# Performance work log

Measured on AMD Instinct MI355X. Metric: run time of the kernel, lower is better.

The kernel has to match this reference:

```python
import jax, jax.numpy as jnp
import numpy as np

B, T, I, H, A = 1024, 2048, 8, 256, 8
DT = 0.1
EPS = 1e-5

def _layernorm(x, g, b):
    m = jnp.mean(x, axis=-1, keepdims=True)
    v = jnp.mean(jnp.square(x - m), axis=-1, keepdims=True)
    return (x - m) * jax.lax.rsqrt(v + EPS) * g + b

def setup_inputs() -> dict:
    key = jax.random.key(0)
    ks = jax.random.split(key, 8)
    xav = float(np.sqrt(6.0 / (H + H)))  # xavier_uniform for rec_weights
    return {
        "x": jax.random.normal(ks[0], (B, T, I), dtype=jnp.float32),
        "W_in": jax.random.normal(ks[1], (I, H), dtype=jnp.float32) * (1.0 / np.sqrt(I)),
        "b_in": jnp.zeros((H,), dtype=jnp.float32),
        "tau_param": jnp.ones((H,), dtype=jnp.float32),
        "W_rec": jax.random.uniform(ks[2], (H, H), dtype=jnp.float32, minval=-xav, maxval=xav),
        "g1": jnp.ones((H,), dtype=jnp.float32),
        "beta1": jnp.zeros((H,), dtype=jnp.float32),
        "g2": jnp.ones((H,), dtype=jnp.float32),
        "beta2": jnp.zeros((H,), dtype=jnp.float32),
        "head_w": jax.random.normal(ks[3], (H, A), dtype=jnp.float32) * (1.0 / np.sqrt(H)),
        "head_b": jnp.zeros((A,), dtype=jnp.float32),
    }

def reference(x, W_in, b_in, tau_param, W_rec, g1, beta1, g2, beta2, head_w, head_b):
    tau = jax.nn.softplus(tau_param)  # [H], broadcast over batch
    # Precompute input projection for all timesteps in one GEMM: [B,T,H]
    u = jnp.einsum("bti,ih->bth", x, W_in) + b_in
    u_t = jnp.swapaxes(u, 0, 1)  # [T,B,H] for scan

    def step(h, u_step):
        f = jnp.tanh(_layernorm(u_step + h @ W_rec, g1, beta1))
        h = jnp.clip(h + (-h / tau + f) * DT, -10.0, 10.0)
        return h, None

    h0 = jnp.zeros((x.shape[0], W_rec.shape[0]), dtype=x.dtype)
    h, _ = jax.lax.scan(step, h0, u_t)
    # per-appliance linear heads, fused into one matmul: [B, A]
    return _layernorm(h, g2, beta2) @ head_w + head_b
```

## Files before the change

### kernel.cpp

```cpp
#include <hip/hip_runtime.h>
#include <hip/hip_bf16.h>

#define T_ 2048
#define B_ 1024
#define H_ 256
#define I_ 8
#define A_ 8
#define DT_ 0.1f
#define EPS_ 1e-5f
#define LSTR 296
#define CH 32
#define RB 8

typedef __attribute__((ext_vector_type(8))) short bf16x8;
typedef __attribute__((ext_vector_type(4))) float f32x4;

#if __has_builtin(__builtin_amdgcn_cvt_pk_bf16_f32)
typedef __attribute__((ext_vector_type(2))) __bf16 bf16x2;
__device__ __forceinline__ int pk2bf(float a, float b) {
    bf16x2 r = __builtin_amdgcn_cvt_pk_bf16_f32(a, b);
    return __builtin_bit_cast(int, r);
}
#else
__device__ __forceinline__ short f2bf1(float f) {
    unsigned u = __builtin_bit_cast(unsigned, f);
    u += 0x7fffu + ((u >> 16) & 1u);
    return (short)(u >> 16);
}
__device__ __forceinline__ int pk2bf(float a, float b) {
    return (int)(unsigned short)f2bf1(a) | ((int)f2bf1(b) << 16);
}
#endif

__launch_bounds__(512, 2)
__global__ void liquid_kernel(const float* __restrict__ x,
                              const float* __restrict__ W_in,
                              const float* __restrict__ b_in,
                              const float* __restrict__ tau_param,
                              const float* __restrict__ W_rec,
                              const float* __restrict__ g1,
                              const float* __restrict__ beta1,
                              const float* __restrict__ g2,
                              const float* __restrict__ beta2,
                              const float* __restrict__ head_w,
                              const float* __restrict__ head_b,
                              float* __restrict__ out) {
    __shared__ short  h_lds[RB * LSTR];
    __shared__ short  xstage[2][CH][RB][8];
    __shared__ alignas(16) int zero16[4];
    __shared__ alignas(16) float2 redt[RB][10];
    __shared__ float  hw[H_ * A_];
    __shared__ float  outp[8][RB][A_];

    const int tid  = threadIdx.x;
    const int w    = tid >> 6;
    const int lane = tid & 63;
    const int quad = lane >> 4;
    const int l15  = lane & 15;
    const int row  = l15 & 7;
    const int half = l15 >> 3;
    const int r0   = blockIdx.x * RB;

    for (int i = tid; i < RB * LSTR; i += 512) h_lds[i] = 0;
    if (tid < 4) zero16[tid] = 0;

    f32x4 pbin0, pbin1;
    float p_g1s[4], p_b1s[4], p_decay[4];
#pragma unroll
    for (int r = 0; r < 4; ++r) {
        pbin0[r] = b_in[w * 32 + quad * 4 + r];
        pbin1[r] = b_in[w * 32 + 16 + quad * 4 + r];
        int c = w * 32 + half * 16 + quad * 4 + r;
        p_g1s[r] = g1[c] * 2.885390082f;
        p_b1s[r] = beta1[c] * 2.885390082f;
        float tp = tau_param[c];
        float sp = (tp > 20.f) ? tp : log1pf(expf(tp));
        p_decay[r] = 1.0f - DT_ / sp;
    }

    bf16x8 afrag[2][9];
#pragma unroll
    for (int mt = 0; mt < 2; ++mt) {
        int cA = w * 32 + mt * 16 + l15;
#pragma unroll
        for (int ks = 0; ks < 9; ++ks) {
            bf16x8 f;
#pragma unroll
            for (int j = 0; j < 8; ++j) {
                int kg = ks * 32 + quad * 8 + j;
                float v;
                if (kg < 256)      v = W_rec[kg * H_ + cA];
                else if (kg < 264) v = W_in[(kg - 256) * H_ + cA];
                else               v = 0.f;
                f[j] = (short)pk2bf(v, v);
            }
            afrag[mt][ks] = f;
        }
    }

    const float* xrbase = x + (size_t)(r0 + w) * T_ * I_;
    const int xt = lane >> 1, xi0 = (lane & 1) * 4;
    float4 xr;

    xr = ((const float4*)xrbase)[lane];
    {
        int2 pk = make_int2(pk2bf(xr.x, xr.y), pk2bf(xr.z, xr.w));
        *reinterpret_cast<int2*>(&xstage[0][xt][w][xi0]) = pk;
    }
    xr = ((const float4*)(xrbase + (size_t)CH * I_))[lane];

    float hreg[4];
#pragma unroll
    for (int s = 0; s < 4; ++s) hreg[s] = 0.f;

    const short* hrow = &h_lds[row * LSTR + quad * 8];
    const f32x4 zacc = {0.f, 0.f, 0.f, 0.f};

    for (int t = 0; t < T_; ++t) {
        const int tc  = t & (CH - 1);
        const int c   = t >> 5;
        const int buf = c & 1;

        __syncthreads();

        if (tc == 16) {
            int2 pk = make_int2(pk2bf(xr.x, xr.y), pk2bf(xr.z, xr.w));
            *reinterpret_cast<int2*>(&xstage[buf ^ 1][xt][w][xi0]) = pk;
        }
        if (tc == 18) {
            int cc = c + 2; if (cc > (T_ / CH) - 1) cc = (T_ / CH) - 1;
            xr = ((const float4*)(xrbase + (size_t)cc * CH * I_))[lane];
        }

        const short* xb = (quad == 0) ? &xstage[buf][tc][row][0] : (const short*)zero16;
        f32x4 c0a = pbin0, c1a = pbin1, c0b = zacc, c1b = zacc;
#pragma unroll
        for (int ks = 0; ks < 4; ++ks) {
            bf16x8 bA = *reinterpret_cast<const bf16x8*>(hrow + ks * 32);
            bf16x8 bB = *reinterpret_cast<const bf16x8*>(hrow + (ks + 4) * 32);
            c0a = __builtin_amdgcn_mfma_f32_16x16x32_bf16(afrag[0][ks],     bA, c0a, 0, 0, 0);
            c1a = __builtin_amdgcn_mfma_f32_16x16x32_bf16(afrag[1][ks],     bA, c1a, 0, 0, 0);
            c0b = __builtin_amdgcn_mfma_f32_16x16x32_bf16(afrag[0][ks + 4], bB, c0b, 0, 0, 0);
            c1b = __builtin_amdgcn_mfma_f32_16x16x32_bf16(afrag[1][ks + 4], bB, c1b, 0, 0, 0);
        }
        {
            bf16x8 b8 = *reinterpret_cast<const bf16x8*>(xb);
            c0a = __builtin_amdgcn_mfma_f32_16x16x32_bf16(afrag[0][8], b8, c0a, 0, 0, 0);
            c1a = __builtin_amdgcn_mfma_f32_16x16x32_bf16(afrag[1][8], b8, c1a, 0, 0, 0);
        }

        f32x4 va;
#pragma unroll
        for (int r = 0; r < 4; ++r) {
            float v0 = c0a[r] + c0b[r];
            float v1 = c1a[r] + c1b[r];
            va[r] = half ? v1 : v0;
        }

        float S  = (va[0] + va[1]) + (va[2] + va[3]);
        float SQ = fmaf(va[0], va[0], fmaf(va[1], va[1],
                   fmaf(va[2], va[2], va[3] * va[3])));
        S += __shfl_xor(S, 8, 64);   SQ += __shfl_xor(SQ, 8, 64);
        S += __shfl_xor(S, 16, 64);  SQ += __shfl_xor(SQ, 16, 64);
        S += __shfl_xor(S, 32, 64);  SQ += __shfl_xor(SQ, 32, 64);
        if (quad == 0 && half == 0) redt[row][w] = make_float2(S, SQ);

        __syncthreads();

        const float4* rrow = reinterpret_cast<const float4*>(&redt[row][0]);
        float4 q0 = rrow[0], q1 = rrow[1], q2 = rrow[2], q3 = rrow[3];
        float St  = ((q0.x + q0.z) + (q1.x + q1.z)) + ((q2.x + q2.z) + (q3.x + q3.z));
        float SQt = ((q0.y + q0.w) + (q1.y + q1.w)) + ((q2.y + q2.w) + (q3.y + q3.w));
        const float mu   = St * (1.f / 256.f);
        const float var  = fmaf(SQt, 1.f / 256.f, -mu * mu);
        const float rstd = __builtin_amdgcn_rsqf(var + EPS_);
        const float nmr  = -mu * rstd;

#pragma unroll
        for (int s = 0; s < 4; ++s) {
            float tt = fmaf(va[s], rstd, nmr);
            float z2 = fmaf(tt, p_g1s[s], p_b1s[s]);
            float e  = __builtin_amdgcn_exp2f(z2);
            float rc = __builtin_amdgcn_rcpf(e + 1.f);
            float fd = fmaf(rc, -2.f * DT_, DT_);
            float h  = fmaf(hreg[s], p_decay[s], fd);
            hreg[s]  = __builtin_amdgcn_fmed3f(h, -10.f, 10.f);
        }
        {
            int2 pk = make_int2(pk2bf(hreg[0], hreg[1]), pk2bf(hreg[2], hreg[3]));
            *reinterpret_cast<int2*>(&h_lds[row * LSTR + w * 32 + half * 16 + quad * 4]) = pk;
        }
    }

    for (int i = tid; i < H_ * A_; i += 512) hw[i] = head_w[i];
    __syncthreads();

    float S2 = (hreg[0] + hreg[1]) + (hreg[2] + hreg[3]);
    float SQ2 = fmaf(hreg[0], hreg[0], fmaf(hreg[1], hreg[1],
                fmaf(hreg[2], hreg[2], hreg[3] * hreg[3])));
    S2 += __shfl_xor(S2, 8, 64);   SQ2 += __shfl_xor(SQ2, 8, 64);
    S2 += __shfl_xor(S2, 16, 64);  SQ2 += __shfl_xor(SQ2, 16, 64);
    S2 += __shfl_xor(S2, 32, 64);  SQ2 += __shfl_xor(SQ2, 32, 64);
    if (quad == 0 && half == 0) redt[row][w] = make_float2(S2, SQ2);
    __syncthreads();
    const float4* rrow = reinterpret_cast<const float4*>(&redt[row][0]);
    float4 q0 = rrow[0], q1 = rrow[1], q2 = rrow[2], q3 = rrow[3];
    float St  = ((q0.x + q0.z) + (q1.x + q1.z)) + ((q2.x + q2.z) + (q3.x + q3.z));
    float SQt = ((q0.y + q0.w) + (q1.y + q1.w)) + ((q2.y + q2.w) + (q3.y + q3.w));
    const float mu   = St * (1.f / 256.f);
    const float var  = fmaf(SQt, 1.f / 256.f, -mu * mu);
    const float rstd = __builtin_amdgcn_rsqf(var + EPS_);

    float pa[8];
#pragma unroll
    for (int a = 0; a < 8; ++a) pa[a] = 0.f;
#pragma unroll
    for (int s = 0; s < 4; ++s) {
        int c = w * 32 + half * 16 + quad * 4 + s;
        float lnh = (hreg[s] - mu) * rstd * g2[c] + beta2[c];
        float4 w0 = *reinterpret_cast<const float4*>(&hw[c * 8]);
        float4 w1 = *reinterpret_cast<const float4*>(&hw[c * 8 + 4]);
        pa[0] += lnh * w0.x; pa[1] += lnh * w0.y; pa[2] += lnh * w0.z; pa[3] += lnh * w0.w;
        pa[4] += lnh * w1.x; pa[5] += lnh * w1.y; pa[6] += lnh * w1.z; pa[7] += lnh * w1.w;
    }
#pragma unroll
    for (int a = 0; a < 8; ++a) {
        pa[a] += __shfl_xor(pa[a], 8, 64);
        pa[a] += __shfl_xor(pa[a], 16, 64);
        pa[a] += __shfl_xor(pa[a], 32, 64);
    }
    if (quad == 0 && half == 0) {
#pragma unroll
        for (int a = 0; a < 8; ++a) outp[w][row][a] = pa[a];
    }
    __syncthreads();
    if (tid < RB * A_) {
        int r = tid >> 3, a = tid & 7;
        float s = head_b[a];
#pragma unroll
        for (int ww = 0; ww < 8; ++ww) s += outp[ww][r][a];
        out[(size_t)(r0 + r) * A_ + a] = s;
    }
}

extern "C" void kernel_launch(void* const* d_in, const int* in_sizes, int n_in,
                              void* d_out, int out_size, void* d_ws, size_t ws_size,
                              hipStream_t stream) {
    const float* x         = (const float*)d_in[0];
    const float* W_in      = (const float*)d_in[1];
    const float* b_in      = (const float*)d_in[2];
    const float* tau_param = (const float*)d_in[3];
    const float* W_rec     = (const float*)d_in[4];
    const float* g1        = (const float*)d_in[5];
    const float* beta1     = (const float*)d_in[6];
    const float* g2        = (const float*)d_in[7];
    const float* beta2     = (const float*)d_in[8];
    const float* head_w    = (const float*)d_in[9];
    const float* head_b    = (const float*)d_in[10];
    float* out = (float*)d_out;

    liquid_kernel<<<128, 512, 0, stream>>>(x, W_in, b_in, tau_param, W_rec,
                                           g1, beta1, g2, beta2, head_w, head_b, out);
}
```

Measured before the change: 1.971 ms.

## Halve rows per block to launch 256 blocks across more CUs

Cuts the batch rows handled per workgroup from 8 to 4 and doubles the grid to 256 blocks, so more compute units each run a shorter per-step serial chain. The MFMA B-fragment now covers 4 rows, with 16 lanes sharing columns. Each thread keeps 2 hidden values instead of 4, and reductions and x staging are remapped to match. The cost is half-empty MFMA columns, since each block still does the full 16-column tile work, plus reworked lane mappings and the per-step block syncs.

```diff
diff --git a/kernel.cpp b/kernel.cpp
--- a/kernel.cpp
+++ b/kernel.cpp
@@ -8,9 +8,9 @@
 #define A_ 8
 #define DT_ 0.1f
 #define EPS_ 1e-5f
-#define LSTR 296
+#define LSTR 304
 #define CH 32
-#define RB 8
+#define RB 4
 
 typedef __attribute__((ext_vector_type(8))) short bf16x8;
 typedef __attribute__((ext_vector_type(4))) float f32x4;
@@ -57,25 +57,30 @@
     const int lane = tid & 63;
     const int quad = lane >> 4;
     const int l15  = lane & 15;
-    const int row  = l15 & 7;
-    const int half = l15 >> 3;
+    const int row  = l15 & 3;
+    const int cj   = l15 >> 2;
+    const int mtj  = cj >> 1;
+    const int rbs  = (cj & 1) * 2;
     const int r0   = blockIdx.x * RB;
 
     for (int i = tid; i < RB * LSTR; i += 512) h_lds[i] = 0;
     if (tid < 4) zero16[tid] = 0;
 
     f32x4 pbin0, pbin1;
-    float p_g1s[4], p_b1s[4], p_decay[4];
+    float p_g1s[2], p_b1s[2], p_decay[2];
 #pragma unroll
     for (int r = 0; r < 4; ++r) {
         pbin0[r] = b_in[w * 32 + quad * 4 + r];
         pbin1[r] = b_in[w * 32 + 16 + quad * 4 + r];
-        int c = w * 32 + half * 16 + quad * 4 + r;
-        p_g1s[r] = g1[c] * 2.885390082f;
-        p_b1s[r] = beta1[c] * 2.885390082f;
+    }
+#pragma unroll
+    for (int s = 0; s < 2; ++s) {
+        int c = w * 32 + mtj * 16 + quad * 4 + rbs + s;
+        p_g1s[s] = g1[c] * 2.885390082f;
+        p_b1s[s] = beta1[c] * 2.885390082f;
         float tp = tau_param[c];
         float sp = (tp > 20.f) ? tp : log1pf(expf(tp));
-        p_decay[r] = 1.0f - DT_ / sp;
+        p_decay[s] = 1.0f - DT_ / sp;
     }
 
     bf16x8 afrag[2][9];
@@ -98,20 +103,21 @@
         }
     }
 
-    const float* xrbase = x + (size_t)(r0 + w) * T_ * I_;
-    const int xt = lane >> 1, xi0 = (lane & 1) * 4;
+    const int xrow = (tid >> 6) & 3, xf4 = tid & 63;
+    const int xt = xf4 >> 1, xi0 = (xf4 & 1) * 4;
+    const bool xldr = (tid < 256);
+    const float* xrbase = x + (size_t)(r0 + xrow) * T_ * I_;
     float4 xr;
 
-    xr = ((const float4*)xrbase)[lane];
-    {
+    if (xldr) {
+        xr = ((const float4*)xrbase)[xf4];
         int2 pk = make_int2(pk2bf(xr.x, xr.y), pk2bf(xr.z, xr.w));
-        *reinterpret_cast<int2*>(&xstage[0][xt][w][xi0]) = pk;
-    }
-    xr = ((const float4*)(xrbase + (size_t)CH * I_))[lane];
-
-    float hreg[4];
-#pragma unroll
-    for (int s = 0; s < 4; ++s) hreg[s] = 0.f;
+        *reinterpret_cast<int2*>(&xstage[0][xt][xrow][xi0]) = pk;
+        xr = ((const float4*)(xrbase + (size_t)CH * I_))[xf4];
+    }
+
+    float hreg[2];
+    hreg[0] = 0.f; hreg[1] = 0.f;
 
     const short* hrow = &h_lds[row * LSTR + quad * 8];
     const f32x4 zacc = {0.f, 0.f, 0.f, 0.f};
@@ -123,13 +129,13 @@
 
         __syncthreads();
 
-        if (tc == 16) {
+        if (xldr && tc == 16) {
             int2 pk = make_int2(pk2bf(xr.x, xr.y), pk2bf(xr.z, xr.w));
-            *reinterpret_cast<int2*>(&xstage[buf ^ 1][xt][w][xi0]) = pk;
-        }
-        if (tc == 18) {
+            *reinterpret_cast<int2*>(&xstage[buf ^ 1][xt][xrow][xi0]) = pk;
+        }
+        if (xldr && tc == 18) {
             int cc = c + 2; if (cc > (T_ / CH) - 1) cc = (T_ / CH) - 1;
-            xr = ((const float4*)(xrbase + (size_t)cc * CH * I_))[lane];
+            xr = ((const float4*)(xrbase + (size_t)cc * CH * I_))[xf4];
         }
 
         const short* xb = (quad == 0) ? &xstage[buf][tc][row][0] : (const short*)zero16;
@@ -148,22 +154,17 @@
             c0a = __builtin_amdgcn_mfma_f32_16x16x32_bf16(afrag[0][8], b8, c0a, 0, 0, 0);
             c1a = __builtin_amdgcn_mfma_f32_16x16x32_bf16(afrag[1][8], b8, c1a, 0, 0, 0);
         }
-
-        f32x4 va;
-#pragma unroll
-        for (int r = 0; r < 4; ++r) {
-            float v0 = c0a[r] + c0b[r];
-            float v1 = c1a[r] + c1b[r];
-            va[r] = half ? v1 : v0;
-        }
-
-        float S  = (va[0] + va[1]) + (va[2] + va[3]);
-        float SQ = fmaf(va[0], va[0], fmaf(va[1], va[1],
-                   fmaf(va[2], va[2], va[3] * va[3])));
-        S += __shfl_xor(S, 8, 64);   SQ += __shfl_xor(SQ, 8, 64);
+        f32x4 acc0 = c0a + c0b, acc1 = c1a + c1b;
+
+        float S  = ((acc0[0] + acc0[1]) + (acc0[2] + acc0[3]))
+                 + ((acc1[0] + acc1[1]) + (acc1[2] + acc1[3]));
+        float SQ = fmaf(acc0[0], acc0[0], fmaf(acc0[1], acc0[1],
+                   fmaf(acc0[2], acc0[2], acc0[3] * acc0[3])))
+                 + fmaf(acc1[0], acc1[0], fmaf(acc1[1], acc1[1],
+                   fmaf(acc1[2], acc1[2], acc1[3] * acc1[3])));
         S += __shfl_xor(S, 16, 64);  SQ += __shfl_xor(SQ, 16, 64);
         S += __shfl_xor(S, 32, 64);  SQ += __shfl_xor(SQ, 32, 64);
-        if (quad == 0 && half == 0) redt[row][w] = make_float2(S, SQ);
+        if (lane < RB) redt[row][w] = make_float2(S, SQ);
 
         __syncthreads();
 
@@ -176,9 +177,11 @@
         const float rstd = __builtin_amdgcn_rsqf(var + EPS_);
         const float nmr  = -mu * rstd;
 
-#pragma unroll
-        for (int s = 0; s < 4; ++s) {
-            float tt = fmaf(va[s], rstd, nmr);
+        f32x4 vsrc = mtj ? acc1 : acc0;
+#pragma unroll
+        for (int s = 0; s < 2; ++s) {
+            float v  = vsrc[rbs + s];
+            float tt = fmaf(v, rstd, nmr);
             float z2 = fmaf(tt, p_g1s[s], p_b1s[s]);
             float e  = __builtin_amdgcn_exp2f(z2);
             float rc = __builtin_amdgcn_rcpf(e + 1.f);
@@ -186,22 +189,20 @@
             float h  = fmaf(hreg[s], p_decay[s], fd);
             hreg[s]  = __builtin_amdgcn_fmed3f(h, -10.f, 10.f);
         }
-        {
-            int2 pk = make_int2(pk2bf(hreg[0], hreg[1]), pk2bf(hreg[2], hreg[3]));
-            *reinterpret_cast<int2*>(&h_lds[row * LSTR + w * 32 + half * 16 + quad * 4]) = pk;
-        }
+        *reinterpret_cast<int*>(&h_lds[row * LSTR + w * 32 + mtj * 16 + quad * 4 + rbs])
+            = pk2bf(hreg[0], hreg[1]);
     }
 
     for (int i = tid; i < H_ * A_; i += 512) hw[i] = head_w[i];
     __syncthreads();
 
-    float S2 = (hreg[0] + hreg[1]) + (hreg[2] + hreg[3]);
-    float SQ2 = fmaf(hreg[0], hreg[0], fmaf(hreg[1], hreg[1],
-                fmaf(hreg[2], hreg[2], hreg[3] * hreg[3])));
+    float S2  = hreg[0] + hreg[1];
+    float SQ2 = fmaf(hreg[0], hreg[0], hreg[1] * hreg[1]);
+    S2 += __shfl_xor(S2, 4, 64);   SQ2 += __shfl_xor(SQ2, 4, 64);
     S2 += __shfl_xor(S2, 8, 64);   SQ2 += __shfl_xor(SQ2, 8, 64);
     S2 += __shfl_xor(S2, 16, 64);  SQ2 += __shfl_xor(SQ2, 16, 64);
     S2 += __shfl_xor(S2, 32, 64);  SQ2 += __shfl_xor(SQ2, 32, 64);
-    if (quad == 0 && half == 0) redt[row][w] = make_float2(S2, SQ2);
+    if (lane < RB) redt[row][w] = make_float2(S2, SQ2);
     __syncthreads();
     const float4* rrow = reinterpret_cast<const float4*>(&redt[row][0]);
     float4 q0 = rrow[0], q1 = rrow[1], q2 = rrow[2], q3 = rrow[3];
@@ -215,21 +216,22 @@
 #pragma unroll
     for (int a = 0; a < 8; ++a) pa[a] = 0.f;
 #pragma unroll
-    for (int s = 0; s < 4; ++s) {
-        int c = w * 32 + half * 16 + quad * 4 + s;
-        float lnh = (hreg[s] - mu) * rstd * g2[c] + beta2[c];
-        float4 w0 = *reinterpret_cast<const float4*>(&hw[c * 8]);
-        float4 w1 = *reinterpret_cast<const float4*>(&hw[c * 8 + 4]);
+    for (int s = 0; s < 2; ++s) {
+        int cc = w * 32 + mtj * 16 + quad * 4 + rbs + s;
+        float lnh = (hreg[s] - mu) * rstd * g2[cc] + beta2[cc];
+        float4 w0 = *reinterpret_cast<const float4*>(&hw[cc * 8]);
+        float4 w1 = *reinterpret_cast<const float4*>(&hw[cc * 8 + 4]);
         pa[0] += lnh * w0.x; pa[1] += lnh * w0.y; pa[2] += lnh * w0.z; pa[3] += lnh * w0.w;
         pa[4] += lnh * w1.x; pa[5] += lnh * w1.y; pa[6] += lnh * w1.z; pa[7] += lnh * w1.w;
     }
 #pragma unroll
     for (int a = 0; a < 8; ++a) {
+        pa[a] += __shfl_xor(pa[a], 4, 64);
         pa[a] += __shfl_xor(pa[a], 8, 64);
         pa[a] += __shfl_xor(pa[a], 16, 64);
         pa[a] += __shfl_xor(pa[a], 32, 64);
     }
-    if (quad == 0 && half == 0) {
+    if (lane < RB) {
 #pragma unroll
         for (int a = 0; a < 8; ++a) outp[w][row][a] = pa[a];
     }
@@ -259,6 +261,6 @@
     const float* head_b    = (const float*)d_in[10];
     float* out = (float*)d_out;
 
-    liquid_kernel<<<128, 512, 0, stream>>>(x, W_in, b_in, tau_param, W_rec,
+    liquid_kernel<<<256, 512, 0, stream>>>(x, W_in, b_in, tau_param, W_rec,
                                            g1, beta1, g2, beta2, head_w, head_b, out);
 }
```

After: 1.771 ms. -10.2%, faster.
